# Kernel tuning notes

Measured on AMD Instinct MI355X. Metric: run time of the kernel, lower is better.

The kernel has to match this reference:

```python
import jax, jax.numpy as jnp
import numpy as np
import math

B, T, C, H = 2, 1024, 768, 12
HD = C // H


def _heads(t):
    # [B,T,C] -> [B,H,T,HD]
    return t.reshape(B, T, H, HD).transpose(0, 2, 1, 3)


def _causal_sdpa(q, k, v):
    # q,k,v: [B,H,T,HD]; scaled dot-product attention with causal mask, no dropout
    scale = 1.0 / math.sqrt(HD)
    s = jnp.einsum('bhqd,bhkd->bhqk', q, k) * scale
    mask = jnp.tril(jnp.ones((T, T), dtype=bool))
    s = jnp.where(mask, s, jnp.finfo(s.dtype).min)
    p = jax.nn.softmax(s, axis=-1)
    return jnp.einsum('bhqk,bhkd->bhqd', p, v)


def setup_inputs() -> dict:
    key = jax.random.key(0)
    k1, k2, k3 = jax.random.split(key, 3)
    x = jax.random.normal(k1, (B, T, C), dtype=jnp.float32)
    eps = 0.1
    x_lower = x - eps
    x_upper = x + eps
    W_attn = jax.random.normal(k2, (3 * C, C), dtype=jnp.float32) * 0.02
    W_proj = jax.random.normal(k3, (C, C), dtype=jnp.float32) * 0.02
    return {'x': x, 'x_lower': x_lower, 'x_upper': x_upper,
            'W_attn': W_attn, 'W_proj': W_proj}


def reference(x, x_lower, x_upper, W_attn, W_proj):
    # main path
    qkv = x @ W_attn.T                       # [B,T,3C]
    q, k, v = jnp.split(qkv, 3, axis=2)
    y = _causal_sdpa(_heads(q), _heads(k), _heads(v))
    y = y.transpose(0, 2, 1, 3).reshape(B, T, C) @ W_proj.T

    # interval bound path (torch runs it under no_grad)
    W_pos = jnp.maximum(W_attn, 0.0)
    W_neg = jnp.minimum(W_attn, 0.0)
    lowers = x_lower @ W_pos.T + x_upper @ W_neg.T   # lower bounds of q,k,v concat
    uppers = x_upper @ W_pos.T + x_lower @ W_neg.T   # upper bounds of q,k,v concat
    qL, kL, vL = (_heads(t) for t in jnp.split(lowers, 3, axis=2))
    qU, kU, vU = (_heads(t) for t in jnp.split(uppers, 3, axis=2))

    y_min = None
    y_max = None
    for qq in (qL, qU):
        for kk in (kL, kU):
            for vv in (vL, vU):
                yb = _causal_sdpa(qq, kk, vv)
                y_min = yb if y_min is None else jnp.minimum(y_min, yb)
                y_max = yb if y_max is None else jnp.maximum(y_max, yb)
    y_lower = y_min.transpose(0, 2, 1, 3).reshape(B, T, C) @ W_proj.T
    y_upper = y_max.transpose(0, 2, 1, 3).reshape(B, T, C) @ W_proj.T
    return (y, y_lower, y_upper)
```

## Files before the change

### kernel.cpp

```cpp
#include <hip/hip_runtime.h>
#include <stdint.h>
#include <math.h>

typedef __attribute__((ext_vector_type(8))) short bf16x8;
typedef __attribute__((ext_vector_type(4))) short s16x4;
typedef __attribute__((ext_vector_type(8))) short s16x8;
typedef __attribute__((ext_vector_type(4))) float f32x4;
typedef __attribute__((ext_vector_type(2))) uint32_t u32x2;

#define DEVI __device__ __forceinline__

constexpr int Bn = 2, Tn = 1024, Cn = 768, Hn = 12, HDn = 64;
constexpr int N3 = 3 * Cn;
constexpr int Mrows = Bn * Tn;
constexpr size_t SZy = (size_t)Mrows * Cn;

template <int V> struct IntC { static constexpr int value = V; };

DEVI short f2bf(float f) {
  union { float f; uint32_t u; } v; v.f = f;
  uint32_t u = v.u;
  return (short)((u + 0x7FFFu + ((u >> 16) & 1u)) >> 16);
}
DEVI float bf2f(short b) {
  union { uint32_t u; float f; } v; v.u = ((uint32_t)(uint16_t)b) << 16;
  return v.f;
}
DEVI float fexp2(float x) { return __builtin_exp2f(x); }
DEVI uint32_t cvtpk(float lo, float hi) {
  uint32_t r;
  asm("v_cvt_pk_bf16_f32 %0, %1, %2" : "=v"(r) : "v"(lo), "v"(hi));
  return r;
}
DEVI void cp16(void* lds, const void* g) {
  __builtin_amdgcn_global_load_lds(
      (const __attribute__((address_space(1))) uint32_t*)(uintptr_t)g,
      (__attribute__((address_space(3))) uint32_t*)(uint32_t)(uintptr_t)lds,
      16, 0, 0);
}
DEVI f32x4 fz() { f32x4 z; z[0] = 0.f; z[1] = 0.f; z[2] = 0.f; z[3] = 0.f; return z; }

__global__ void prep_x(const float* __restrict__ x, const float* __restrict__ xl,
                       const float* __restrict__ xu, short* __restrict__ xb,
                       short* __restrict__ mb, short* __restrict__ rb) {
  int i = blockIdx.x * 256 + threadIdx.x;
  float4 vx = ((const float4*)x)[i];
  float4 vl = ((const float4*)xl)[i];
  float4 vu = ((const float4*)xu)[i];
  s16x4 a, m_, g;
  a[0] = f2bf(vx.x); a[1] = f2bf(vx.y); a[2] = f2bf(vx.z); a[3] = f2bf(vx.w);
  m_[0] = f2bf(0.5f * (vl.x + vu.x)); m_[1] = f2bf(0.5f * (vl.y + vu.y));
  m_[2] = f2bf(0.5f * (vl.z + vu.z)); m_[3] = f2bf(0.5f * (vl.w + vu.w));
  g[0] = f2bf(0.5f * (vu.x - vl.x)); g[1] = f2bf(0.5f * (vu.y - vl.y));
  g[2] = f2bf(0.5f * (vu.z - vl.z)); g[3] = f2bf(0.5f * (vu.w - vl.w));
  ((s16x4*)xb)[i] = a; ((s16x4*)mb)[i] = m_; ((s16x4*)rb)[i] = g;
}
__global__ void prep_wall(const float* __restrict__ Wa, const float* __restrict__ Wp,
                          short* __restrict__ wb, short* __restrict__ awb,
                          short* __restrict__ wpb) {
  const int bid = blockIdx.x;
  if (bid < 1728) {
    int i = bid * 256 + threadIdx.x;
    float4 v = ((const float4*)Wa)[i];
    s16x4 a, b2;
    a[0] = f2bf(v.x); a[1] = f2bf(v.y); a[2] = f2bf(v.z); a[3] = f2bf(v.w);
    b2[0] = f2bf(fabsf(v.x)); b2[1] = f2bf(fabsf(v.y));
    b2[2] = f2bf(fabsf(v.z)); b2[3] = f2bf(fabsf(v.w));
    ((s16x4*)wb)[i] = a; ((s16x4*)awb)[i] = b2;
  } else {
    int i = (bid - 1728) * 256 + threadIdx.x;
    float4 v = ((const float4*)Wp)[i];
    s16x4 a;
    a[0] = f2bf(v.x); a[1] = f2bf(v.y); a[2] = f2bf(v.z); a[3] = f2bf(v.w);
    ((s16x4*)wpb)[i] = a;
  }
}

__launch_bounds__(256, 3)
__global__ void gemm_qkv3(const short* __restrict__ A0, const short* __restrict__ A1,
                          const short* __restrict__ A2, const short* __restrict__ B0,
                          const short* __restrict__ B1, short* __restrict__ qkv,
                          short* __restrict__ low, short* __restrict__ up) {
  constexpr int BM = 64, BN = 128;
  __shared__ short At[3 * BM * 32];
  __shared__ short Bt[2 * BN * 32];
  const int tid = threadIdx.x, wave = tid >> 6, lane = tid & 63;
  const int g = lane >> 4, q = lane & 15;
  const int wm = wave >> 1, wn = wave & 1;
  const int brow = blockIdx.x * BM, bcol = blockIdx.y * BN;
  const short* As[3] = {A0, A1, A2};
  const short* Bs[2] = {B0, B1};

  f32x4 acc[3][2][4];
#pragma unroll
  for (int a = 0; a < 3; a++)
#pragma unroll
    for (int m = 0; m < 2; m++)
#pragma unroll
      for (int n = 0; n < 4; n++) acc[a][m][n] = fz();

  const int arow = tid >> 2, ac = tid & 3;
  for (int kt = 0; kt < Cn / 32; ++kt) {
#pragma unroll
    for (int a = 0; a < 3; a++)
      cp16((char*)At + a * 4096 + tid * 16,
           As[a] + (size_t)(brow + arow) * Cn + (kt * 32 + ac * 8));
#pragma unroll
    for (int b2 = 0; b2 < 2; b2++)
#pragma unroll
      for (int ii = 0; ii < 2; ++ii) {
        int i = wave * 2 + ii;
        int ch = i * 64 + lane, row = ch >> 2, c = ch & 3;
        cp16((char*)Bt + b2 * 8192 + i * 1024,
             Bs[b2] + (size_t)(bcol + row) * Cn + (kt * 32 + c * 8));
      }
    __syncthreads();
    bf16x8 bfr[2][4];
#pragma unroll
    for (int b2 = 0; b2 < 2; b2++)
#pragma unroll
      for (int n = 0; n < 4; n++) {
        int r = wn * 64 + n * 16 + q;
        bfr[b2][n] = *(const bf16x8*)&Bt[b2 * (BN * 32) + r * 32 + g * 8];
      }
#pragma unroll
    for (int a = 0; a < 3; a++) {
      bf16x8 af[2];
#pragma unroll
      for (int m = 0; m < 2; m++) {
        int r = wm * 32 + m * 16 + q;
        af[m] = *(const bf16x8*)&At[a * (BM * 32) + r * 32 + g * 8];
      }
      const int bs = (a == 2) ? 1 : 0;
#pragma unroll
      for (int m = 0; m < 2; m++)
#pragma unroll
        for (int n = 0; n < 4; n++)
          acc[a][m][n] = __builtin_amdgcn_mfma_f32_16x16x32_bf16(
              af[m], bfr[bs][n], acc[a][m][n], 0, 0, 0);
    }
    __syncthreads();
  }
#pragma unroll
  for (int m = 0; m < 2; m++)
#pragma unroll
    for (int n = 0; n < 4; n++)
#pragma unroll
      for (int r = 0; r < 4; r++) {
        int row = brow + wm * 32 + m * 16 + g * 4 + r;
        int col = bcol + wn * 64 + n * 16 + q;
        size_t idx = (size_t)row * N3 + col;
        float v0 = acc[0][m][n][r], v1 = acc[1][m][n][r], v2 = acc[2][m][n][r];
        qkv[idx] = f2bf(v0);
        low[idx] = f2bf(v1 - v2);
        up[idx]  = f2bf(v1 + v2);
      }
}

__launch_bounds__(256, 4)
__global__ void gemm_proj(const short* __restrict__ A0, const short* __restrict__ A1,
                          const short* __restrict__ A2, const short* __restrict__ Bw,
                          float* __restrict__ out) {
  constexpr int BM = 64, BN = 128;
  __shared__ short At[BM * 32];
  __shared__ short Bt[BN * 32];
  const short* Ap = blockIdx.z == 0 ? A0 : (blockIdx.z == 1 ? A1 : A2);
  float* op = out + (size_t)blockIdx.z * SZy;
  const int tid = threadIdx.x, wave = tid >> 6, lane = tid & 63;
  const int wm = wave >> 1, wn = wave & 1;
  const int brow = blockIdx.x * BM, bcol = blockIdx.y * BN;

  f32x4 acc[2][4];
#pragma unroll
  for (int m = 0; m < 2; m++)
#pragma unroll
    for (int n = 0; n < 4; n++) acc[m][n] = fz();

  const int chunk = wave * 64 + lane, srow = chunk >> 2, sc = chunk & 3;
  for (int kt = 0; kt < Cn / 32; ++kt) {
    cp16((char*)At + wave * 1024, Ap + (size_t)(brow + srow) * Cn + (kt * 32 + sc * 8));
#pragma unroll
    for (int ii = 0; ii < 2; ++ii) {
      int i = wave * 2 + ii;
      int ch = i * 64 + lane, row = ch >> 2, c = ch & 3;
      cp16((char*)Bt + i * 1024, Bw + (size_t)(bcol + row) * Cn + (kt * 32 + c * 8));
    }
    __syncthreads();
    bf16x8 af[2], bfr[4];
#pragma unroll
    for (int m = 0; m < 2; m++) {
      int r = wm * 32 + m * 16 + (lane & 15);
      af[m] = *(const bf16x8*)&At[r * 32 + (lane >> 4) * 8];
    }
#pragma unroll
    for (int n = 0; n < 4; n++) {
      int r = wn * 64 + n * 16 + (lane & 15);
      bfr[n] = *(const bf16x8*)&Bt[r * 32 + (lane >> 4) * 8];
    }
#pragma unroll
    for (int m = 0; m < 2; m++)
#pragma unroll
      for (int n = 0; n < 4; n++)
        acc[m][n] = __builtin_amdgcn_mfma_f32_16x16x32_bf16(af[m], bfr[n], acc[m][n], 0, 0, 0);
    __syncthreads();
  }
#pragma unroll
  for (int m = 0; m < 2; m++)
#pragma unroll
    for (int n = 0; n < 4; n++)
#pragma unroll
      for (int r = 0; r < 4; r++) {
        int row = brow + wm * 32 + m * 16 + (lane >> 4) * 4 + r;
        int col = bcol + wn * 64 + n * 16 + (lane & 15);
        op[(size_t)row * Cn + col] = acc[m][n][r];
      }
}

__global__ void vtrans(const short* __restrict__ s0, const short* __restrict__ s1,
                       const short* __restrict__ s2, short* __restrict__ d0,
                       short* __restrict__ d1, short* __restrict__ d2) {
  __shared__ short tile[64][72];
  const short* src = blockIdx.z == 0 ? s0 : (blockIdx.z == 1 ? s1 : s2);
  short* dst = blockIdx.z == 0 ? d0 : (blockIdx.z == 1 ? d1 : d2);
  const int tt = blockIdx.x, bh = blockIdx.y;
  const int b = bh / Hn, h = bh % Hn;
  const int tid = threadIdx.x;
#pragma unroll
  for (int i = 0; i < 2; i++) {
    int chunk = i * 256 + tid;
    int t = chunk >> 3, c = chunk & 7;
    s16x8 v = *(const s16x8*)(src + (size_t)(b * Tn + tt * 64 + t) * N3 +
                              2 * Cn + h * HDn + c * 8);
    *(s16x8*)&tile[t][c * 8] = v;
  }
  __syncthreads();
#pragma unroll
  for (int i = 0; i < 2; i++) {
    int chunk = i * 256 + tid;
    int d = chunk >> 3, tc = chunk & 7;
    s16x8 v;
#pragma unroll
    for (int j = 0; j < 8; j++) v[j] = tile[tc * 8 + j][d];
    *(s16x8*)(dst + (size_t)bh * (64 * 1024) + (size_t)d * 1024 + tt * 64 + tc * 8) = v;
  }
}

__launch_bounds__(256, 3)
__global__ void flash_all(const short* __restrict__ qkv, const short* __restrict__ lowb,
                          const short* __restrict__ upb, const short* __restrict__ vtq,
                          const short* __restrict__ vtl, const short* __restrict__ vtu,
                          short* __restrict__ yab, short* __restrict__ comb) {
  constexpr float SCL = 0.18033688f;
  constexpr float THR = 8.0f / SCL;
  __shared__ short Kt[64 * 64];
  __shared__ short Vt0[64 * 64];
  __shared__ short Vt1[64 * 64];
  __shared__ short Pt[8 * 16 * 64];
  const int tid = threadIdx.x, wave = tid >> 6, lane = tid & 63;
  const int g = lane >> 4, q = lane & 15;
  const int bh = blockIdx.x, combo = blockIdx.y;
  const int j = 7 - blockIdx.z;
  const int qt0 = j * 128;
  const int b = bh / Hn, h = bh % Hn;
  const bool isMain = (combo == 4);
  const short* Qsrc = isMain ? qkv : ((combo & 2) ? upb : lowb);
  const short* Ksrc = isMain ? qkv : ((combo & 1) ? upb : lowb);
  const short* V0t = isMain ? vtq : vtl;
  const short* V1t = vtu;
  const int qswz = (q & 7) << 4;

  int koff[2], voff[2];
#pragma unroll
  for (int ii = 0; ii < 2; ++ii) {
    int chunk = (wave * 2 + ii) * 64 + lane, row = chunk >> 3, c = chunk & 7;
    int cg = c ^ (row & 7);
    koff[ii] = row * N3 + cg * 8;
    voff[ii] = row * 1024 + cg * 8;
  }
  const short* Kbase = Ksrc + (size_t)(b * Tn) * N3 + Cn + h * HDn;
  const short* V0base = V0t + (size_t)bh * (64 * 1024);
  const short* V1base = V1t + (size_t)bh * (64 * 1024);

  bf16x8 aq[2][2];
#pragma unroll
  for (int u = 0; u < 2; u++) {
    int trow = qt0 + u * 64 + wave * 16 + q;
    const short* qp = Qsrc + (size_t)(b * Tn + trow) * N3 + h * HDn;
#pragma unroll
    for (int s = 0; s < 2; s++) aq[u][s] = *(const bf16x8*)(qp + s * 32 + g * 8);
  }

  f32x4 o0[2][4], o1[2][4];
  float mrow[2], lrow[2];
#pragma unroll
  for (int u = 0; u < 2; u++) {
    mrow[u] = -INFINITY; lrow[u] = 0.f;
#pragma unroll
    for (int n = 0; n < 4; n++) { o0[u][n] = fz(); o1[u][n] = fz(); }
  }

  auto softmax_u = [&](f32x4 (&sv)[4], int u, auto diagc) {
    constexpr bool DIAG = decltype(diagc)::value;
    if constexpr (DIAG) {
      const int rhs = wave * 16 + q, kb = g * 4;
#pragma unroll
      for (int m = 0; m < 4; m++)
#pragma unroll
        for (int r = 0; r < 4; r++)
          sv[m][r] = (m * 16 + kb + r <= rhs) ? sv[m][r] : -INFINITY;
    }
    float mx = -INFINITY;
#pragma unroll
    for (int m = 0; m < 4; m++)
#pragma unroll
      for (int r = 0; r < 4; r++) mx = fmaxf(mx, sv[m][r]);
    mx = fmaxf(mx, __shfl_xor(mx, 16));
    mx = fmaxf(mx, __shfl_xor(mx, 32));
    if (!__all(mx <= mrow[u] + THR)) {
      float mnew = fmaxf(mrow[u], mx);
      float corr = fexp2((mrow[u] - mnew) * SCL);
      mrow[u] = mnew; lrow[u] *= corr;
#pragma unroll
      for (int n = 0; n < 4; n++) {
        o0[u][n][0] *= corr; o0[u][n][1] *= corr;
        o0[u][n][2] *= corr; o0[u][n][3] *= corr;
      }
      if (!isMain) {
#pragma unroll
        for (int n = 0; n < 4; n++) {
          o1[u][n][0] *= corr; o1[u][n][1] *= corr;
          o1[u][n][2] *= corr; o1[u][n][3] *= corr;
        }
      }
    }
    const float nms = -mrow[u] * SCL;
    float ps = 0.f;
#pragma unroll
    for (int m = 0; m < 4; m++)
#pragma unroll
      for (int r = 0; r < 4; r++) {
        float p = fexp2(fmaf(sv[m][r], SCL, nms));
        sv[m][r] = p;
        ps += p;
      }
    ps += __shfl_xor(ps, 16);
    ps += __shfl_xor(ps, 32);
    lrow[u] += ps;
    char* PtW = (char*)Pt + (wave * 2 + u) * 2048;
#pragma unroll
    for (int m = 0; m < 4; m++) {
      u32x2 w;
      w[0] = cvtpk(sv[m][0], sv[m][1]);
      w[1] = cvtpk(sv[m][2], sv[m][3]);
      *(u32x2*)(PtW + ((q * 128 + m * 32 + g * 8) ^ qswz)) = w;
    }
  };

  auto kv_iter = [&](int kv, auto m0c, auto m1c) {
    constexpr int M0 = decltype(m0c)::value;
    constexpr int M1 = decltype(m1c)::value;
#pragma unroll
    for (int ii = 0; ii < 2; ++ii)
      cp16((char*)Kt + (wave * 2 + ii) * 1024, Kbase + (size_t)kv * (64 * N3) + koff[ii]);
#pragma unroll
    for (int ii = 0; ii < 2; ++ii)
      cp16((char*)Vt0 + (wave * 2 + ii) * 1024, V0base + kv * 64 + voff[ii]);
    if (!isMain) {
#pragma unroll
      for (int ii = 0; ii < 2; ++ii)
        cp16((char*)Vt1 + (wave * 2 + ii) * 1024, V1base + kv * 64 + voff[ii]);
    }
    __syncthreads();

    f32x4 sa0[4], sa1[4];
#pragma unroll
    for (int m = 0; m < 4; m++) { sa0[m] = fz(); sa1[m] = fz(); }
    __builtin_amdgcn_s_setprio(1);
#pragma unroll
    for (int m = 0; m < 4; m++) {
#pragma unroll
      for (int s = 0; s < 2; s++) {
        int krow = m * 16 + q;
        bf16x8 bk = *(const bf16x8*)((char*)Kt +
            krow * 128 + ((g * 16 + s * 64) ^ ((krow & 7) << 4)));
        if constexpr (M0 > 0)
          sa0[m] = __builtin_amdgcn_mfma_f32_16x16x32_bf16(bk, aq[0][s], sa0[m], 0, 0, 0);
        if constexpr (M1 > 0)
          sa1[m] = __builtin_amdgcn_mfma_f32_16x16x32_bf16(bk, aq[1][s], sa1[m], 0, 0, 0);
      }
    }
    __builtin_amdgcn_s_setprio(0);

    if constexpr (M0 > 0) softmax_u(sa0, 0, IntC<(M0 == 1)>{});
    if constexpr (M1 > 0) softmax_u(sa1, 1, IntC<(M1 == 1)>{});

    __builtin_amdgcn_s_setprio(1);
#pragma unroll
    for (int kk = 0; kk < 2; kk++) {
      bf16x8 pb0, pb1;
      if constexpr (M0 > 0)
        pb0 = *(const bf16x8*)((char*)Pt + (wave * 2 + 0) * 2048 +
                               ((q * 128 + kk * 64 + g * 16) ^ qswz));
      if constexpr (M1 > 0)
        pb1 = *(const bf16x8*)((char*)Pt + (wave * 2 + 1) * 2048 +
                               ((q * 128 + kk * 64 + g * 16) ^ qswz));
#pragma unroll
      for (int mf = 0; mf < 4; mf++) {
        int drow = mf * 16 + q;
        int boff = drow * 128 + ((g * 16 + kk * 64) ^ ((drow & 7) << 4));
        bf16x8 av0 = *(const bf16x8*)((char*)Vt0 + boff);
        if constexpr (M0 > 0)
          o0[0][mf] = __builtin_amdgcn_mfma_f32_16x16x32_bf16(av0, pb0, o0[0][mf], 0, 0, 0);
        if constexpr (M1 > 0)
          o0[1][mf] = __builtin_amdgcn_mfma_f32_16x16x32_bf16(av0, pb1, o0[1][mf], 0, 0, 0);
        if (!isMain) {
          bf16x8 av1 = *(const bf16x8*)((char*)Vt1 + boff);
          if constexpr (M0 > 0)
            o1[0][mf] = __builtin_amdgcn_mfma_f32_16x16x32_bf16(av1, pb0, o1[0][mf], 0, 0, 0);
          if constexpr (M1 > 0)
            o1[1][mf] = __builtin_amdgcn_mfma_f32_16x16x32_bf16(av1, pb1, o1[1][mf], 0, 0, 0);
        }
      }
    }
    __builtin_amdgcn_s_setprio(0);
    __syncthreads();
  };

  const int jj = 2 * j;
  for (int kv = 0; kv < jj; ++kv) kv_iter(kv, IntC<2>{}, IntC<2>{});
  kv_iter(jj, IntC<1>{}, IntC<2>{});
  kv_iter(jj + 1, IntC<0>{}, IntC<1>{});

#pragma unroll
  for (int u = 0; u < 2; u++) {
    const float inv = 1.0f / lrow[u];
    const int trow = qt0 + u * 64 + wave * 16 + q;
    const size_t rowbase = (size_t)(b * Tn + trow) * Cn + h * HDn + g * 4;
#pragma unroll
    for (int mf = 0; mf < 4; mf++) {
      size_t idx = rowbase + mf * 16;
      u32x2 v0;
      v0[0] = cvtpk(o0[u][mf][0] * inv, o0[u][mf][1] * inv);
      v0[1] = cvtpk(o0[u][mf][2] * inv, o0[u][mf][3] * inv);
      if (isMain) {
        *(u32x2*)(yab + idx) = v0;
      } else {
        u32x2 v1;
        v1[0] = cvtpk(o1[u][mf][0] * inv, o1[u][mf][1] * inv);
        v1[1] = cvtpk(o1[u][mf][2] * inv, o1[u][mf][3] * inv);
        *(u32x2*)(comb + (size_t)(2 * combo) * SZy + idx) = v0;
        *(u32x2*)(comb + (size_t)(2 * combo + 1) * SZy + idx) = v1;
      }
    }
  }
}

__global__ void reduce_minmax(const short* __restrict__ comb, short* __restrict__ ymn,
                              short* __restrict__ ymx) {
  int i = blockIdx.x * 256 + threadIdx.x;
  s16x8 mn8 = ((const s16x8*)(comb + 0 * SZy))[i];
  s16x8 mx8 = ((const s16x8*)(comb + 1 * SZy))[i];
#pragma unroll
  for (int c = 1; c < 4; c++) {
    s16x8 a = ((const s16x8*)(comb + (size_t)(2 * c) * SZy))[i];
    s16x8 b2 = ((const s16x8*)(comb + (size_t)(2 * c + 1) * SZy))[i];
#pragma unroll
    for (int j = 0; j < 8; j++) {
      mn8[j] = f2bf(fminf(bf2f(mn8[j]), bf2f(a[j])));
      mx8[j] = f2bf(fmaxf(bf2f(mx8[j]), bf2f(b2[j])));
    }
  }
  ((s16x8*)ymn)[i] = mn8;
  ((s16x8*)ymx)[i] = mx8;
}

extern "C" void kernel_launch(void* const* d_in, const int* in_sizes, int n_in,
                              void* d_out, int out_size, void* d_ws, size_t ws_size,
                              hipStream_t stream) {
  const float* x  = (const float*)d_in[0];
  const float* xl = (const float*)d_in[1];
  const float* xu = (const float*)d_in[2];
  const float* Wa = (const float*)d_in[3];
  const float* Wp = (const float*)d_in[4];
  float* out = (float*)d_out;

  char* p = (char*)d_ws;
  auto carve = [&](size_t bytes) -> char* {
    char* r = p; p += (bytes + 255) & ~(size_t)255; return r;
  };
  short* xb   = (short*)carve((size_t)Mrows * Cn * 2);
  short* midb = (short*)carve((size_t)Mrows * Cn * 2);
  short* radb = (short*)carve((size_t)Mrows * Cn * 2);
  short* wb   = (short*)carve((size_t)N3 * Cn * 2);
  short* awb  = (short*)carve((size_t)N3 * Cn * 2);
  short* wpb  = (short*)carve((size_t)Cn * Cn * 2);
  short* qkvb = (short*)carve((size_t)Mrows * N3 * 2);
  short* lowb = (short*)carve((size_t)Mrows * N3 * 2);
  short* upb  = (short*)carve((size_t)Mrows * N3 * 2);
  short* vtq  = (short*)carve((size_t)24 * 64 * 1024 * 2);
  short* vtl  = (short*)carve((size_t)24 * 64 * 1024 * 2);
  short* vtu  = (short*)carve((size_t)24 * 64 * 1024 * 2);
  short* yab  = (short*)carve(SZy * 2);
  short* ymnb = (short*)carve(SZy * 2);
  short* ymxb = (short*)carve(SZy * 2);
  short* comb = (short*)carve(8 * SZy * 2);

  prep_x<<<1536, 256, 0, stream>>>(x, xl, xu, xb, midb, radb);
  prep_wall<<<2304, 256, 0, stream>>>(Wa, Wp, wb, awb, wpb);

  gemm_qkv3<<<dim3(32, 18), 256, 0, stream>>>(xb, midb, radb, wb, awb,
                                              qkvb, lowb, upb);

  vtrans<<<dim3(16, 24, 3), 256, 0, stream>>>(qkvb, lowb, upb, vtq, vtl, vtu);

  flash_all<<<dim3(24, 5, 8), 256, 0, stream>>>(qkvb, lowb, upb, vtq, vtl, vtu,
                                                yab, comb);

  reduce_minmax<<<768, 256, 0, stream>>>(comb, ymnb, ymxb);

  gemm_proj<<<dim3(32, 6, 3), 256, 0, stream>>>(yab, ymnb, ymxb, wpb, out);
}
```

Baseline: 130.1 us.

## Double-buffer K tiles in LDS and load V fragments directly into registers

The flash attention kernel now double-buffers the K tile in shared memory, prefetching the next KV block's K with async global-to-LDS copies while the current block is computed. V fragments are no longer staged through LDS; each lane reads its MFMA operands for V0 and V1 straight from the pre-transposed global V buffers. This is meant to hide K load latency and cut LDS traffic and footprint. In exchange it adds more uncoalesced-ish global reads per wave and more register pressure from holding V fragments, which may hurt occupancy.

```diff
diff --git a/kernel.cpp b/kernel.cpp
--- a/kernel.cpp
+++ b/kernel.cpp
@@ -39,6 +39,10 @@
       16, 0, 0);
 }
 DEVI f32x4 fz() { f32x4 z; z[0] = 0.f; z[1] = 0.f; z[2] = 0.f; z[3] = 0.f; return z; }
+DEVI void wait_all() {
+  asm volatile("s_waitcnt vmcnt(0) lgkmcnt(0)" ::: "memory");
+  __builtin_amdgcn_sched_barrier(0);
+}
 
 __global__ void prep_x(const float* __restrict__ x, const float* __restrict__ xl,
                        const float* __restrict__ xu, short* __restrict__ xb,
@@ -252,9 +256,7 @@
                           short* __restrict__ yab, short* __restrict__ comb) {
   constexpr float SCL = 0.18033688f;
   constexpr float THR = 8.0f / SCL;
-  __shared__ short Kt[64 * 64];
-  __shared__ short Vt0[64 * 64];
-  __shared__ short Vt1[64 * 64];
+  __shared__ short Kt[2][64 * 64];
   __shared__ short Pt[8 * 16 * 64];
   const int tid = threadIdx.x, wave = tid >> 6, lane = tid & 63;
   const int g = lane >> 4, q = lane & 15;
@@ -268,18 +270,21 @@
   const short* V0t = isMain ? vtq : vtl;
   const short* V1t = vtu;
   const int qswz = (q & 7) << 4;
-
-  int koff[2], voff[2];
+  const int jjmax = 2 * j + 1;
+
+  int koff[2];
 #pragma unroll
   for (int ii = 0; ii < 2; ++ii) {
     int chunk = (wave * 2 + ii) * 64 + lane, row = chunk >> 3, c = chunk & 7;
     int cg = c ^ (row & 7);
     koff[ii] = row * N3 + cg * 8;
-    voff[ii] = row * 1024 + cg * 8;
   }
   const short* Kbase = Ksrc + (size_t)(b * Tn) * N3 + Cn + h * HDn;
   const short* V0base = V0t + (size_t)bh * (64 * 1024);
   const short* V1base = V1t + (size_t)bh * (64 * 1024);
+  int voffr[4];
+#pragma unroll
+  for (int mf = 0; mf < 4; mf++) voffr[mf] = (mf * 16 + q) * 1024 + g * 8;
 
   bf16x8 aq[2][2];
 #pragma unroll
@@ -356,21 +361,28 @@
     }
   };
 
-  auto kv_iter = [&](int kv, auto m0c, auto m1c) {
+#pragma unroll
+  for (int ii = 0; ii < 2; ++ii)
+    cp16((char*)Kt[0] + (wave * 2 + ii) * 1024, Kbase + koff[ii]);
+  wait_all();
+  __builtin_amdgcn_s_barrier();
+
+  auto kv_iter = [&](int kv, int p, auto m0c, auto m1c) {
     constexpr int M0 = decltype(m0c)::value;
     constexpr int M1 = decltype(m1c)::value;
-#pragma unroll
-    for (int ii = 0; ii < 2; ++ii)
-      cp16((char*)Kt + (wave * 2 + ii) * 1024, Kbase + (size_t)kv * (64 * N3) + koff[ii]);
-#pragma unroll
-    for (int ii = 0; ii < 2; ++ii)
-      cp16((char*)Vt0 + (wave * 2 + ii) * 1024, V0base + kv * 64 + voff[ii]);
-    if (!isMain) {
+    bf16x8 vf0[2][4];
+#pragma unroll
+    for (int kk = 0; kk < 2; kk++)
+#pragma unroll
+      for (int mf = 0; mf < 4; mf++)
+        vf0[kk][mf] = *(const bf16x8*)(V0base + voffr[mf] + kv * 64 + kk * 32);
+    {
+      int kvn = kv + 1 > jjmax ? jjmax : kv + 1;
 #pragma unroll
       for (int ii = 0; ii < 2; ++ii)
-        cp16((char*)Vt1 + (wave * 2 + ii) * 1024, V1base + kv * 64 + voff[ii]);
-    }
-    __syncthreads();
+        cp16((char*)Kt[p ^ 1] + (wave * 2 + ii) * 1024,
+             Kbase + (size_t)kvn * (64 * N3) + koff[ii]);
+    }
 
     f32x4 sa0[4], sa1[4];
 #pragma unroll
@@ -381,7 +393,7 @@
 #pragma unroll
       for (int s = 0; s < 2; s++) {
         int krow = m * 16 + q;
-        bf16x8 bk = *(const bf16x8*)((char*)Kt +
+        bf16x8 bk = *(const bf16x8*)((char*)Kt[p] +
             krow * 128 + ((g * 16 + s * 64) ^ ((krow & 7) << 4)));
         if constexpr (M0 > 0)
           sa0[m] = __builtin_amdgcn_mfma_f32_16x16x32_bf16(bk, aq[0][s], sa0[m], 0, 0, 0);
@@ -393,6 +405,15 @@
 
     if constexpr (M0 > 0) softmax_u(sa0, 0, IntC<(M0 == 1)>{});
     if constexpr (M1 > 0) softmax_u(sa1, 1, IntC<(M1 == 1)>{});
+
+    bf16x8 vf1[2][4];
+    if (!isMain) {
+#pragma unroll
+      for (int kk = 0; kk < 2; kk++)
+#pragma unroll
+        for (int mf = 0; mf < 4; mf++)
+          vf1[kk][mf] = *(const bf16x8*)(V1base + voffr[mf] + kv * 64 + kk * 32);
+    }
 
     __builtin_amdgcn_s_setprio(1);
 #pragma unroll
@@ -406,30 +427,28 @@
                                ((q * 128 + kk * 64 + g * 16) ^ qswz));
 #pragma unroll
       for (int mf = 0; mf < 4; mf++) {
-        int drow = mf * 16 + q;
-        int boff = drow * 128 + ((g * 16 + kk * 64) ^ ((drow & 7) << 4));
-        bf16x8 av0 = *(const bf16x8*)((char*)Vt0 + boff);
         if constexpr (M0 > 0)
-          o0[0][mf] = __builtin_amdgcn_mfma_f32_16x16x32_bf16(av0, pb0, o0[0][mf], 0, 0, 0);
+          o0[0][mf] = __builtin_amdgcn_mfma_f32_16x16x32_bf16(vf0[kk][mf], pb0, o0[0][mf], 0, 0, 0);
         if constexpr (M1 > 0)
-          o0[1][mf] = __builtin_amdgcn_mfma_f32_16x16x32_bf16(av0, pb1, o0[1][mf], 0, 0, 0);
+          o0[1][mf] = __builtin_amdgcn_mfma_f32_16x16x32_bf16(vf0[kk][mf], pb1, o0[1][mf], 0, 0, 0);
         if (!isMain) {
-          bf16x8 av1 = *(const bf16x8*)((char*)Vt1 + boff);
           if constexpr (M0 > 0)
-            o1[0][mf] = __builtin_amdgcn_mfma_f32_16x16x32_bf16(av1, pb0, o1[0][mf], 0, 0, 0);
+            o1[0][mf] = __builtin_amdgcn_mfma_f32_16x16x32_bf16(vf1[kk][mf], pb0, o1[0][mf], 0, 0, 0);
           if constexpr (M1 > 0)
-            o1[1][mf] = __builtin_amdgcn_mfma_f32_16x16x32_bf16(av1, pb1, o1[1][mf], 0, 0, 0);
+            o1[1][mf] = __builtin_amdgcn_mfma_f32_16x16x32_bf16(vf1[kk][mf], pb1, o1[1][mf], 0, 0, 0);
         }
       }
     }
     __builtin_amdgcn_s_setprio(0);
-    __syncthreads();
+    wait_all();
+    __builtin_amdgcn_s_barrier();
   };
 
   const int jj = 2 * j;
-  for (int kv = 0; kv < jj; ++kv) kv_iter(kv, IntC<2>{}, IntC<2>{});
-  kv_iter(jj, IntC<1>{}, IntC<2>{});
-  kv_iter(jj + 1, IntC<0>{}, IntC<1>{});
+  int p = 0;
+  for (int kv = 0; kv < jj; ++kv) { kv_iter(kv, p, IntC<2>{}, IntC<2>{}); p ^= 1; }
+  kv_iter(jj, p, IntC<1>{}, IntC<2>{}); p ^= 1;
+  kv_iter(jj + 1, p, IntC<0>{}, IntC<1>{});
 
 #pragma unroll
   for (int u = 0; u < 2; u++) {
```

Result: slower. 241.1 us (+85.4%).
